# Performance work log

Measured on AMD Instinct MI355X. Metric: run time of the kernel, lower is better.

## Reference

```python
import jax, jax.numpy as jnp
import numpy as np

N_NODES = 100000
N_EDGES = 1600000
IN_FEATS = 128
HIDDEN = 128


def _graph_conv(x, W, b, src, dst, n_nodes):
    # DGL GraphConv with norm='both': out = D_in^{-1/2} * A^T * (D_out^{-1/2} * x) @ W + b
    ones = jnp.ones((src.shape[0],), dtype=x.dtype)
    deg_out = jax.ops.segment_sum(ones, src, num_segments=n_nodes)
    deg_in = jax.ops.segment_sum(ones, dst, num_segments=n_nodes)
    norm_src = jax.lax.rsqrt(jnp.clip(deg_out, 1.0))  # [N]
    norm_dst = jax.lax.rsqrt(jnp.clip(deg_in, 1.0))   # [N]
    h = x @ W                                          # [N, F_out]
    msg = h[src] * norm_src[src][:, None]              # gather by edge src: [E, F_out]
    agg = jax.ops.segment_sum(msg, dst, num_segments=n_nodes)  # scatter-add to dst
    return agg * norm_dst[:, None] + b


def setup_inputs() -> dict:
    key = jax.random.key(0)
    ks = jax.random.split(key, 9)
    x = jax.random.normal(ks[0], (N_NODES, IN_FEATS), dtype=jnp.float32)
    src = jax.random.randint(ks[1], (N_EDGES,), 0, N_NODES, dtype=jnp.int32)
    dst = jax.random.randint(ks[2], (N_EDGES,), 0, N_NODES, dtype=jnp.int32)
    s1 = 1.0 / np.sqrt(IN_FEATS)
    s2 = 1.0 / np.sqrt(HIDDEN)
    W1 = jax.random.uniform(ks[3], (IN_FEATS, HIDDEN), jnp.float32, -s1, s1)
    b1 = jnp.zeros((HIDDEN,), jnp.float32)
    W2 = jax.random.uniform(ks[4], (HIDDEN, HIDDEN), jnp.float32, -s2, s2)
    b2 = jnp.zeros((HIDDEN,), jnp.float32)
    sp = 1.0 / np.sqrt(2 * HIDDEN)
    Wp = jax.random.uniform(ks[5], (2 * HIDDEN, 1), jnp.float32, -sp, sp)
    bp = jax.random.uniform(ks[6], (1,), jnp.float32, -sp, sp)
    return {"x": x, "W1": W1, "b1": b1, "W2": W2, "b2": b2,
            "Wp": Wp, "bp": bp, "src": src, "dst": dst}


def reference(x, W1, b1, W2, b2, Wp, bp, src, dst):
    n_nodes = x.shape[0]
    h = _graph_conv(x, W1, b1, src, dst, n_nodes)
    h = jax.nn.relu(h)
    h = _graph_conv(h, W2, b2, src, dst, n_nodes)  # final node embeddings [N, H]
    # predict_links on the same edge list: cat(h[u], h[v]) -> linear -> sigmoid
    edge_h = jnp.concatenate([h[src], h[dst]], axis=1)  # [E, 2H]
    scores = jax.nn.sigmoid(edge_h @ Wp + bp)           # [E, 1]
    return scores
```

## Files before the change

kernel.cpp:

```cpp
#include <hip/hip_runtime.h>
#include <cstdint>
#include <cstddef>

#define NN 100000
#define NE 1600000
#define F  128
#define NPAD 100352
#define NBUCK 782
#define BCAPG 2560
#define CHUNK 4167

typedef __attribute__((ext_vector_type(8))) short bf16x8;
typedef __attribute__((ext_vector_type(4))) float f32x4;

__device__ __forceinline__ unsigned short f2bf(float f) {
    unsigned u = __float_as_uint(f);
    unsigned r = (u + 0x7fffu + ((u >> 16) & 1u)) >> 16;
    return (unsigned short)r;
}
__device__ __forceinline__ void acc_bf8s(const uint4 v, const float ns, float* acc) {
    acc[0] += __uint_as_float(v.x << 16) * ns;
    acc[1] += __uint_as_float(v.x & 0xffff0000u) * ns;
    acc[2] += __uint_as_float(v.y << 16) * ns;
    acc[3] += __uint_as_float(v.y & 0xffff0000u) * ns;
    acc[4] += __uint_as_float(v.z << 16) * ns;
    acc[5] += __uint_as_float(v.z & 0xffff0000u) * ns;
    acc[6] += __uint_as_float(v.w << 16) * ns;
    acc[7] += __uint_as_float(v.w & 0xffff0000u) * ns;
}

__global__ void setup_kernel(int* __restrict__ gCur,
                             const float* __restrict__ W2, const float* __restrict__ Wp,
                             const float* __restrict__ b2, const float* __restrict__ bp,
                             float* __restrict__ consts, float2* __restrict__ V) {
    const int g = blockIdx.x;
    const int tid = threadIdx.x;
    if (g < 4) {
        const int b = g * 256 + tid;
        if (b < NBUCK) gCur[b] = b * BCAPG;
        return;
    }
    if (tid < 128) {
        float sa = 0.f, sc = 0.f;
        #pragma unroll 8
        for (int j = 0; j < F; ++j) {
            const float w = W2[tid * F + j];
            sa += w * Wp[j];
            sc += w * Wp[F + j];
        }
        V[tid] = make_float2(sa, sc);
    } else if (tid < 192) {
        const int l = tid - 128;
        const float2 bb = *(const float2*)&b2[2 * l];
        const float2 wa = *(const float2*)&Wp[2 * l];
        const float2 wc = *(const float2*)&Wp[F + 2 * l];
        float s = bb.x * (wa.x + wc.x) + bb.y * (wa.y + wc.y);
        #pragma unroll
        for (int m = 32; m > 0; m >>= 1) s += __shfl_xor(s, m);
        if (l == 0) consts[0] = s + bp[0];
    }
}

__global__ __launch_bounds__(256, 3)
void gemm1_fill_kernel(const float* __restrict__ in, const float* __restrict__ W,
                       unsigned short* __restrict__ out_bf,
                       const int* __restrict__ src, const int* __restrict__ dst,
                       int* __restrict__ deg_out, int* __restrict__ gCur,
                       int* __restrict__ srcPart) {
    __shared__ __align__(16) char smem[31264];

    const int g = blockIdx.x;
    const int tid = threadIdx.x;

    if (g & 1) {
        int* packedL = (int*)smem;
        unsigned short* bktL = (unsigned short*)(packedL + CHUNK);
        int* hist = (int*)((char*)smem + 25008);
        int* curL = hist + NBUCK;
        const int e0 = (g >> 1) * CHUNK;
        const int nCh = min(CHUNK, NE - e0);
        for (int i = tid; i < NBUCK; i += 256) hist[i] = 0;
        __syncthreads();
        for (int i = tid; i < nCh; i += 256) {
            const int s = src[e0 + i];
            const int d = dst[e0 + i];
            atomicAdd(&deg_out[s], 1);
            const int bkt = d >> 7;
            atomicAdd(&hist[bkt], 1);
            packedL[i] = s | ((d & 127) << 17);
            bktL[i] = (unsigned short)bkt;
        }
        __syncthreads();
        for (int b = tid; b < NBUCK; b += 256) {
            const int c = hist[b];
            curL[b] = (c > 0) ? atomicAdd(&gCur[b], c) : 0;
        }
        __syncthreads();
        for (int i = tid; i < nCh; i += 256) {
            const int bkt = bktL[i];
            const int p = atomicAdd(&curL[bkt], 1);
            if (p < (bkt + 1) * BCAPG)
                srcPart[p] = packedL[i];
        }
        return;
    }

    char* A_s = smem;

    const int gid  = g >> 1;
    const int w    = tid >> 6;
    const int lane = tid & 63;
    const int ml   = lane & 15;
    const int quad = lane >> 4;

    bf16x8 Bf[4][2];
    #pragma unroll
    for (int kb = 0; kb < 4; ++kb) {
        #pragma unroll
        for (int nb = 0; nb < 2; ++nb) {
            const int n = 32 * w + nb * 16 + ml;
            const int k0 = kb * 32 + quad * 8;
            #pragma unroll
            for (int j = 0; j < 8; ++j)
                Bf[kb][nb][j] = (short)f2bf(W[(k0 + j) * F + n]);
        }
    }

    const int nTiles = NN / 32;
    for (int tile = gid; tile < nTiles; tile += 384) {
        const int row0 = tile * 32;
        __syncthreads();
        #pragma unroll
        for (int c = 0; c < 2; ++c) {
            const int i2 = tid + 256 * c;
            const int m  = i2 >> 4;
            const int o  = i2 & 15;
            const float* xr = &in[(size_t)(row0 + m) * F + o * 8];
            const float4 v0 = *(const float4*)xr;
            const float4 v1 = *(const float4*)(xr + 4);
            short h8[8];
            h8[0] = (short)f2bf(v0.x); h8[1] = (short)f2bf(v0.y);
            h8[2] = (short)f2bf(v0.z); h8[3] = (short)f2bf(v0.w);
            h8[4] = (short)f2bf(v1.x); h8[5] = (short)f2bf(v1.y);
            h8[6] = (short)f2bf(v1.z); h8[7] = (short)f2bf(v1.w);
            const int kb2 = o >> 2, q2 = o & 3, ml2 = m & 15, mh2 = m >> 4;
            const int fo = (((mh2 * 4 + kb2) * 64) + q2 * 16 + ml2) * 16;
            *(bf16x8*)(A_s + fo) = *(bf16x8*)h8;
        }
        __syncthreads();

        f32x4 acc00 = {0,0,0,0}, acc01 = {0,0,0,0}, acc10 = {0,0,0,0}, acc11 = {0,0,0,0};
        #pragma unroll
        for (int kb = 0; kb < 4; ++kb) {
            const bf16x8 ah0 = *(const bf16x8*)(A_s + (kb * 64 + lane) * 16);
            const bf16x8 ah1 = *(const bf16x8*)(A_s + ((4 + kb) * 64 + lane) * 16);
            acc00 = __builtin_amdgcn_mfma_f32_16x16x32_bf16(ah0, Bf[kb][0], acc00, 0, 0, 0);
            acc01 = __builtin_amdgcn_mfma_f32_16x16x32_bf16(ah0, Bf[kb][1], acc01, 0, 0, 0);
            acc10 = __builtin_amdgcn_mfma_f32_16x16x32_bf16(ah1, Bf[kb][0], acc10, 0, 0, 0);
            acc11 = __builtin_amdgcn_mfma_f32_16x16x32_bf16(ah1, Bf[kb][1], acc11, 0, 0, 0);
        }

        #pragma unroll
        for (int mh = 0; mh < 2; ++mh) {
            #pragma unroll
            for (int nb = 0; nb < 2; ++nb) {
                const f32x4 a = (mh == 0) ? (nb == 0 ? acc00 : acc01)
                                          : (nb == 0 ? acc10 : acc11);
                const int row = row0 + mh * 16 + quad * 4;
                const int col = 32 * w + nb * 16 + ml;
                #pragma unroll
                for (int r = 0; r < 4; ++r)
                    out_bf[(size_t)(row + r) * F + col] = f2bf(a[r]);
            }
        }
    }
}

__global__ void normsrc_kernel(const int* __restrict__ deg_out, float* __restrict__ norm_src, int nN) {
    const int n = blockIdx.x * blockDim.x + threadIdx.x;
    if (n < nN) norm_src[n] = rsqrtf((float)max(deg_out[n], 1));
}

__global__ __launch_bounds__(256)
void gather_sort_kernel(const unsigned short* __restrict__ hs,
                        int* __restrict__ srcPart, const int* __restrict__ gCur,
                        const float* __restrict__ norm_src, const float* __restrict__ bias,
                        const float2* __restrict__ V, float2* __restrict__ uw,
                        int* __restrict__ offs, int* __restrict__ ends,
                        float* __restrict__ norm_dst) {
    __shared__ int cnt[128];
    __shared__ int loc[128];
    __shared__ int cur[128];
    __shared__ int sortedL[BCAPG];

    const int b   = blockIdx.x;
    const int tid = threadIdx.x;
    const int nlo = b * 128;
    const int nCnt = min(128, NN - nlo);
    const int eBase = b * BCAPG;
    const int total = min(gCur[b] - eBase, BCAPG);

    if (tid < 128) cnt[tid] = 0;
    __syncthreads();
    for (int i = tid; i < total; i += 256)
        atomicAdd(&cnt[(srcPart[eBase + i] >> 17) & 127], 1);
    __syncthreads();
    if (tid < 128) loc[tid] = cnt[tid];
    __syncthreads();
    for (int off = 1; off < 128; off <<= 1) {
        int v = 0;
        if (tid < 128 && tid >= off) v = loc[tid - off];
        __syncthreads();
        if (tid < 128) loc[tid] += v;
        __syncthreads();
    }
    if (tid < 128) cur[tid] = loc[tid] - cnt[tid];
    if (tid < nCnt) {
        const int st = eBase + loc[tid] - cnt[tid];
        offs[nlo + tid] = st;
        ends[nlo + tid] = st + cnt[tid];
        norm_dst[nlo + tid] = rsqrtf((float)max(cnt[tid], 1));
    }
    __syncthreads();
    for (int i = tid; i < total; i += 256) {
        const int v = srcPart[eBase + i];
        const int r = atomicAdd(&cur[(v >> 17) & 127], 1);
        sortedL[r] = v & 0x1FFFF;
    }
    __syncthreads();
    for (int i = tid; i < total; i += 256)
        srcPart[eBase + i] = sortedL[i];

    const int w  = tid >> 6;
    const int l  = tid & 63;
    const int q  = l >> 4;
    const int c8 = (l & 15) * 8;
    float bb[8];
    *(float4*)&bb[0] = *(const float4*)&bias[c8];
    *(float4*)&bb[4] = *(const float4*)&bias[c8 + 4];
    float2 Vl[8];
    #pragma unroll
    for (int k = 0; k < 8; ++k) Vl[k] = V[c8 + k];

    const int nhEnd = min((w + 1) * 32, nCnt);
    for (int nh = w * 32; nh < nhEnd; ++nh) {
        const int end = loc[nh];
        const int beg = end - cnt[nh];
        float acc[8] = {0.f, 0.f, 0.f, 0.f, 0.f, 0.f, 0.f, 0.f};
        int j = beg;
        for (; j + 16 <= end; j += 16) {
            const int s0 = sortedL[j + q];
            const int s1 = sortedL[j + 4 + q];
            const int s2 = sortedL[j + 8 + q];
            const int s3 = sortedL[j + 12 + q];
            const float ns0 = norm_src[s0];
            const float ns1 = norm_src[s1];
            const float ns2 = norm_src[s2];
            const float ns3 = norm_src[s3];
            const uint4 v0 = *(const uint4*)&hs[(size_t)s0 * F + c8];
            const uint4 v1 = *(const uint4*)&hs[(size_t)s1 * F + c8];
            const uint4 v2 = *(const uint4*)&hs[(size_t)s2 * F + c8];
            const uint4 v3 = *(const uint4*)&hs[(size_t)s3 * F + c8];
            acc_bf8s(v0, ns0, acc);
            acc_bf8s(v1, ns1, acc);
            acc_bf8s(v2, ns2, acc);
            acc_bf8s(v3, ns3, acc);
        }
        for (; j + 8 <= end; j += 8) {
            const int s0 = sortedL[j + q];
            const int s1 = sortedL[j + 4 + q];
            const float ns0 = norm_src[s0];
            const float ns1 = norm_src[s1];
            const uint4 v0 = *(const uint4*)&hs[(size_t)s0 * F + c8];
            const uint4 v1 = *(const uint4*)&hs[(size_t)s1 * F + c8];
            acc_bf8s(v0, ns0, acc);
            acc_bf8s(v1, ns1, acc);
        }
        for (; j + 4 <= end; j += 4) {
            const int s = sortedL[j + q];
            const float ns = norm_src[s];
            const uint4 v = *(const uint4*)&hs[(size_t)s * F + c8];
            acc_bf8s(v, ns, acc);
        }
        if (j + q < end) {
            const int s = sortedL[j + q];
            const float ns = norm_src[s];
            const uint4 v = *(const uint4*)&hs[(size_t)s * F + c8];
            acc_bf8s(v, ns, acc);
        }
        #pragma unroll
        for (int k = 0; k < 8; ++k) {
            acc[k] += __shfl_xor(acc[k], 16);
            acc[k] += __shfl_xor(acc[k], 32);
        }

        const int n = nlo + nh;
        const float nd = rsqrtf((float)max(cnt[nh], 1));
        float pa = 0.f, pc = 0.f;
        #pragma unroll
        for (int k = 0; k < 8; ++k) {
            const float ok = fmaxf(acc[k] * nd + bb[k], 0.f);
            pa += ok * Vl[k].x;
            pc += ok * Vl[k].y;
        }
        #pragma unroll
        for (int m = 1; m <= 8; m <<= 1) {
            pa += __shfl_xor(pa, m);
            pc += __shfl_xor(pc, m);
        }
        if (l == 0) {
            const float ns = norm_src[n];
            uw[n] = make_float2(ns * pa, ns * pc);
        }
    }
}

__global__ void ac_kernel(const float2* __restrict__ uw, const int* __restrict__ sorted_src,
                          const int* __restrict__ offs, const int* __restrict__ ends,
                          const float* __restrict__ norm_dst,
                          float* __restrict__ A, float* __restrict__ C, int nN) {
    const int n = blockIdx.x * blockDim.x + threadIdx.x;
    if (n >= nN) return;
    const int beg = offs[n];
    const int end = ends[n];
    float su = 0.f, sw = 0.f;
    int j = beg;
    for (; j + 2 <= end; j += 2) {
        const float2 t0 = uw[sorted_src[j]];
        const float2 t1 = uw[sorted_src[j + 1]];
        su += t0.x + t1.x;
        sw += t0.y + t1.y;
    }
    if (j < end) {
        const float2 t = uw[sorted_src[j]];
        su += t.x;
        sw += t.y;
    }
    const float nd = norm_dst[n];
    A[n] = nd * su;
    C[n] = nd * sw;
}

__global__ void score_kernel(const float* __restrict__ A, const float* __restrict__ C,
                             const int4* __restrict__ src4, const int4* __restrict__ dst4,
                             const float* __restrict__ consts, float4* __restrict__ out4,
                             int nE4) {
    const int i = blockIdx.x * blockDim.x + threadIdx.x;
    if (i < nE4) {
        const int4 s = src4[i];
        const int4 d = dst4[i];
        const float cc = consts[0];
        float4 o;
        o.x = 1.f / (1.f + __expf(-(A[s.x] + C[d.x] + cc)));
        o.y = 1.f / (1.f + __expf(-(A[s.y] + C[d.y] + cc)));
        o.z = 1.f / (1.f + __expf(-(A[s.z] + C[d.z] + cc)));
        o.w = 1.f / (1.f + __expf(-(A[s.w] + C[d.w] + cc)));
        out4[i] = o;
    }
}

extern "C" void kernel_launch(void* const* d_in, const int* in_sizes, int n_in,
                              void* d_out, int out_size, void* d_ws, size_t ws_size,
                              hipStream_t stream) {
    const float* x  = (const float*)d_in[0];
    const float* W1 = (const float*)d_in[1];
    const float* b1 = (const float*)d_in[2];
    const float* W2 = (const float*)d_in[3];
    const float* b2 = (const float*)d_in[4];
    const float* Wp = (const float*)d_in[5];
    const float* bp = (const float*)d_in[6];
    const int*   src = (const int*)d_in[7];
    const int*   dst = (const int*)d_in[8];
    float* out = (float*)d_out;

    float* ws        = (float*)d_ws;
    float* norm_src  = ws;
    float* bufA      = ws + NPAD;
    float* bufC      = ws + 2 * NPAD;
    float* norm_dst  = ws + 3 * NPAD;
    int*   offs      = (int*)(ws + 4 * NPAD);
    int*   ends      = offs + NPAD;
    int*   gCur      = ends + NPAD;
    float* consts    = (float*)(gCur + 1024);
    float2* V        = (float2*)(consts + 16);
    float2* uw       = V + 128;
    int*   srcPart   = (int*)(uw + NN);
    unsigned short* hs_bf = (unsigned short*)(srcPart + (size_t)NBUCK * BCAPG);

    hipMemsetAsync(bufA, 0, NPAD * sizeof(int), stream);
    setup_kernel<<<5, 256, 0, stream>>>(gCur, W2, Wp, b2, bp, consts, V);

    gemm1_fill_kernel<<<768, 256, 0, stream>>>(x, W1, hs_bf, src, dst,
                                               (int*)bufA, gCur, srcPart);

    normsrc_kernel<<<(NN + 255) / 256, 256, 0, stream>>>((const int*)bufA, norm_src, NN);

    gather_sort_kernel<<<NBUCK, 256, 0, stream>>>(hs_bf, srcPart, gCur, norm_src, b1,
                                                  V, uw, offs, ends, norm_dst);

    ac_kernel<<<(NN + 255) / 256, 256, 0, stream>>>(uw, srcPart, offs, ends, norm_dst,
                                                    bufA, bufC, NN);

    score_kernel<<<(NE / 4 + 255) / 256, 256, 0, stream>>>(bufA, bufC, (const int4*)src,
                                                           (const int4*)dst, consts,
                                                           (float4*)out, NE / 4);
}
```

Measured before the change: 312.9 us.

## Drop normsrc kernel, rebalance fill/GEMM blocks, parallelize ac per node

Removes the separate norm_src kernel by computing rsqrt of out-degree inline in the gather kernel. gCur is now zeroed by the existing memset, so the setup kernel no longer initializes it. The fused GEMM/fill kernel changes its block split from 1:1 to 1 GEMM to 2 fill blocks with smaller edge chunks. The ac kernel now uses 8 lanes per node with a shuffle reduction, giving more parallelism for the irregular gathers. Together these cut a launch and shift work balance, at the cost of recomputing rsqrt per edge and putting fewer blocks on the GEMM.

```diff
diff --git a/kernel.cpp b/kernel.cpp
--- a/kernel.cpp
+++ b/kernel.cpp
@@ -8,7 +8,7 @@
 #define NPAD 100352
 #define NBUCK 782
 #define BCAPG 2560
-#define CHUNK 4167
+#define CHUNK 3125
 
 typedef __attribute__((ext_vector_type(8))) short bf16x8;
 typedef __attribute__((ext_vector_type(4))) float f32x4;
@@ -28,18 +28,14 @@
     acc[6] += __uint_as_float(v.w << 16) * ns;
     acc[7] += __uint_as_float(v.w & 0xffff0000u) * ns;
 }
-
-__global__ void setup_kernel(int* __restrict__ gCur,
-                             const float* __restrict__ W2, const float* __restrict__ Wp,
+__device__ __forceinline__ float deg2norm(int d) {
+    return rsqrtf((float)max(d, 1));
+}
+
+__global__ void setup_kernel(const float* __restrict__ W2, const float* __restrict__ Wp,
                              const float* __restrict__ b2, const float* __restrict__ bp,
                              float* __restrict__ consts, float2* __restrict__ V) {
-    const int g = blockIdx.x;
     const int tid = threadIdx.x;
-    if (g < 4) {
-        const int b = g * 256 + tid;
-        if (b < NBUCK) gCur[b] = b * BCAPG;
-        return;
-    }
     if (tid < 128) {
         float sa = 0.f, sc = 0.f;
         #pragma unroll 8
@@ -67,17 +63,19 @@
                        const int* __restrict__ src, const int* __restrict__ dst,
                        int* __restrict__ deg_out, int* __restrict__ gCur,
                        int* __restrict__ srcPart) {
-    __shared__ __align__(16) char smem[31264];
+    __shared__ __align__(16) char smem[25008];
 
     const int g = blockIdx.x;
+    const int r3 = g % 3;
     const int tid = threadIdx.x;
 
-    if (g & 1) {
+    if (r3 != 0) {
         int* packedL = (int*)smem;
         unsigned short* bktL = (unsigned short*)(packedL + CHUNK);
-        int* hist = (int*)((char*)smem + 25008);
+        int* hist = (int*)(smem + 18752);
         int* curL = hist + NBUCK;
-        const int e0 = (g >> 1) * CHUNK;
+        const int fid = (g / 3) * 2 + (r3 - 1);
+        const int e0 = fid * CHUNK;
         const int nCh = min(CHUNK, NE - e0);
         for (int i = tid; i < NBUCK; i += 256) hist[i] = 0;
         __syncthreads();
@@ -93,7 +91,7 @@
         __syncthreads();
         for (int b = tid; b < NBUCK; b += 256) {
             const int c = hist[b];
-            curL[b] = (c > 0) ? atomicAdd(&gCur[b], c) : 0;
+            curL[b] = (c > 0) ? (b * BCAPG + atomicAdd(&gCur[b], c)) : 0;
         }
         __syncthreads();
         for (int i = tid; i < nCh; i += 256) {
@@ -107,7 +105,7 @@
 
     char* A_s = smem;
 
-    const int gid  = g >> 1;
+    const int gid  = g / 3;
     const int w    = tid >> 6;
     const int lane = tid & 63;
     const int ml   = lane & 15;
@@ -127,7 +125,7 @@
     }
 
     const int nTiles = NN / 32;
-    for (int tile = gid; tile < nTiles; tile += 384) {
+    for (int tile = gid; tile < nTiles; tile += 256) {
         const int row0 = tile * 32;
         __syncthreads();
         #pragma unroll
@@ -176,15 +174,10 @@
     }
 }
 
-__global__ void normsrc_kernel(const int* __restrict__ deg_out, float* __restrict__ norm_src, int nN) {
-    const int n = blockIdx.x * blockDim.x + threadIdx.x;
-    if (n < nN) norm_src[n] = rsqrtf((float)max(deg_out[n], 1));
-}
-
 __global__ __launch_bounds__(256)
 void gather_sort_kernel(const unsigned short* __restrict__ hs,
                         int* __restrict__ srcPart, const int* __restrict__ gCur,
-                        const float* __restrict__ norm_src, const float* __restrict__ bias,
+                        const int* __restrict__ deg_out, const float* __restrict__ bias,
                         const float2* __restrict__ V, float2* __restrict__ uw,
                         int* __restrict__ offs, int* __restrict__ ends,
                         float* __restrict__ norm_dst) {
@@ -198,7 +191,7 @@
     const int nlo = b * 128;
     const int nCnt = min(128, NN - nlo);
     const int eBase = b * BCAPG;
-    const int total = min(gCur[b] - eBase, BCAPG);
+    const int total = min(gCur[b], BCAPG);
 
     if (tid < 128) cnt[tid] = 0;
     __syncthreads();
@@ -219,7 +212,7 @@
         const int st = eBase + loc[tid] - cnt[tid];
         offs[nlo + tid] = st;
         ends[nlo + tid] = st + cnt[tid];
-        norm_dst[nlo + tid] = rsqrtf((float)max(cnt[tid], 1));
+        norm_dst[nlo + tid] = deg2norm(cnt[tid]);
     }
     __syncthreads();
     for (int i = tid; i < total; i += 256) {
@@ -253,10 +246,10 @@
             const int s1 = sortedL[j + 4 + q];
             const int s2 = sortedL[j + 8 + q];
             const int s3 = sortedL[j + 12 + q];
-            const float ns0 = norm_src[s0];
-            const float ns1 = norm_src[s1];
-            const float ns2 = norm_src[s2];
-            const float ns3 = norm_src[s3];
+            const float ns0 = deg2norm(deg_out[s0]);
+            const float ns1 = deg2norm(deg_out[s1]);
+            const float ns2 = deg2norm(deg_out[s2]);
+            const float ns3 = deg2norm(deg_out[s3]);
             const uint4 v0 = *(const uint4*)&hs[(size_t)s0 * F + c8];
             const uint4 v1 = *(const uint4*)&hs[(size_t)s1 * F + c8];
             const uint4 v2 = *(const uint4*)&hs[(size_t)s2 * F + c8];
@@ -269,8 +262,8 @@
         for (; j + 8 <= end; j += 8) {
             const int s0 = sortedL[j + q];
             const int s1 = sortedL[j + 4 + q];
-            const float ns0 = norm_src[s0];
-            const float ns1 = norm_src[s1];
+            const float ns0 = deg2norm(deg_out[s0]);
+            const float ns1 = deg2norm(deg_out[s1]);
             const uint4 v0 = *(const uint4*)&hs[(size_t)s0 * F + c8];
             const uint4 v1 = *(const uint4*)&hs[(size_t)s1 * F + c8];
             acc_bf8s(v0, ns0, acc);
@@ -278,13 +271,13 @@
         }
         for (; j + 4 <= end; j += 4) {
             const int s = sortedL[j + q];
-            const float ns = norm_src[s];
+            const float ns = deg2norm(deg_out[s]);
             const uint4 v = *(const uint4*)&hs[(size_t)s * F + c8];
             acc_bf8s(v, ns, acc);
         }
         if (j + q < end) {
             const int s = sortedL[j + q];
-            const float ns = norm_src[s];
+            const float ns = deg2norm(deg_out[s]);
             const uint4 v = *(const uint4*)&hs[(size_t)s * F + c8];
             acc_bf8s(v, ns, acc);
         }
@@ -295,7 +288,7 @@
         }
 
         const int n = nlo + nh;
-        const float nd = rsqrtf((float)max(cnt[nh], 1));
+        const float nd = deg2norm(cnt[nh]);
         float pa = 0.f, pc = 0.f;
         #pragma unroll
         for (int k = 0; k < 8; ++k) {
@@ -309,7 +302,7 @@
             pc += __shfl_xor(pc, m);
         }
         if (l == 0) {
-            const float ns = norm_src[n];
+            const float ns = deg2norm(deg_out[n]);
             uw[n] = make_float2(ns * pa, ns * pc);
         }
     }
@@ -319,26 +312,26 @@
                           const int* __restrict__ offs, const int* __restrict__ ends,
                           const float* __restrict__ norm_dst,
                           float* __restrict__ A, float* __restrict__ C, int nN) {
-    const int n = blockIdx.x * blockDim.x + threadIdx.x;
+    const int gid = blockIdx.x * blockDim.x + threadIdx.x;
+    const int n   = gid >> 3;
     if (n >= nN) return;
+    const int sub = gid & 7;
     const int beg = offs[n];
     const int end = ends[n];
     float su = 0.f, sw = 0.f;
-    int j = beg;
-    for (; j + 2 <= end; j += 2) {
-        const float2 t0 = uw[sorted_src[j]];
-        const float2 t1 = uw[sorted_src[j + 1]];
-        su += t0.x + t1.x;
-        sw += t0.y + t1.y;
-    }
-    if (j < end) {
+    for (int j = beg + sub; j < end; j += 8) {
         const float2 t = uw[sorted_src[j]];
         su += t.x;
         sw += t.y;
     }
-    const float nd = norm_dst[n];
-    A[n] = nd * su;
-    C[n] = nd * sw;
+    su += __shfl_xor(su, 1); sw += __shfl_xor(sw, 1);
+    su += __shfl_xor(su, 2); sw += __shfl_xor(sw, 2);
+    su += __shfl_xor(su, 4); sw += __shfl_xor(sw, 4);
+    if (sub == 0) {
+        const float nd = norm_dst[n];
+        A[n] = nd * su;
+        C[n] = nd * sw;
+    }
 }
 
 __global__ void score_kernel(const float* __restrict__ A, const float* __restrict__ C,
@@ -374,32 +367,29 @@
     float* out = (float*)d_out;
 
     float* ws        = (float*)d_ws;
-    float* norm_src  = ws;
-    float* bufA      = ws + NPAD;
-    float* bufC      = ws + 2 * NPAD;
-    float* norm_dst  = ws + 3 * NPAD;
-    int*   offs      = (int*)(ws + 4 * NPAD);
+    float* bufA      = ws;
+    int*   gCur      = (int*)(ws + NPAD);
+    float* bufC      = ws + NPAD + 1024;
+    float* norm_dst  = bufC + NPAD;
+    int*   offs      = (int*)(norm_dst + NPAD);
     int*   ends      = offs + NPAD;
-    int*   gCur      = ends + NPAD;
-    float* consts    = (float*)(gCur + 1024);
+    float* consts    = (float*)(ends + NPAD);
     float2* V        = (float2*)(consts + 16);
     float2* uw       = V + 128;
     int*   srcPart   = (int*)(uw + NN);
     unsigned short* hs_bf = (unsigned short*)(srcPart + (size_t)NBUCK * BCAPG);
 
-    hipMemsetAsync(bufA, 0, NPAD * sizeof(int), stream);
-    setup_kernel<<<5, 256, 0, stream>>>(gCur, W2, Wp, b2, bp, consts, V);
+    hipMemsetAsync(bufA, 0, (NPAD + 1024) * sizeof(int), stream);
+    setup_kernel<<<1, 256, 0, stream>>>(W2, Wp, b2, bp, consts, V);
 
     gemm1_fill_kernel<<<768, 256, 0, stream>>>(x, W1, hs_bf, src, dst,
                                                (int*)bufA, gCur, srcPart);
 
-    normsrc_kernel<<<(NN + 255) / 256, 256, 0, stream>>>((const int*)bufA, norm_src, NN);
-
-    gather_sort_kernel<<<NBUCK, 256, 0, stream>>>(hs_bf, srcPart, gCur, norm_src, b1,
+    gather_sort_kernel<<<NBUCK, 256, 0, stream>>>(hs_bf, srcPart, gCur, (const int*)bufA, b1,
                                                   V, uw, offs, ends, norm_dst);
 
-    ac_kernel<<<(NN + 255) / 256, 256, 0, stream>>>(uw, srcPart, offs, ends, norm_dst,
-                                                    bufA, bufC, NN);
+    ac_kernel<<<(NN * 8 + 255) / 256, 256, 0, stream>>>(uw, srcPart, offs, ends, norm_dst,
+                                                        bufA, bufC, NN);
 
     score_kernel<<<(NE / 4 + 255) / 256, 256, 0, stream>>>(bufA, bufC, (const int4*)src,
                                                            (const int4*)dst, consts,
```

Result: no change. 312.9 us (+0.0%).
